# Performance work log

Measured on AMD Instinct MI355X. Metric: run time of the kernel, lower is better.

Reference implementation:

```python
import math
import jax, jax.numpy as jnp
import numpy as np

B, S, D_MODEL = 4, 1024, 512
D_BAR, C_ONSET, N_HEADS = 256, 32, 8
T_ONSET, POOL = 8192, 8


def setup_inputs() -> dict:
    key = jax.random.key(0)
    ks = jax.random.split(key, 16)
    p = lambda i, shape: jax.random.normal(ks[i], shape, dtype=jnp.float32) * 0.05
    return {
        "token_embs": jax.random.normal(ks[0], (B, S, D_MODEL), dtype=jnp.float32),
        "onset_1d": jax.random.uniform(ks[1], (B, T_ONSET, C_ONSET), dtype=jnp.float32),
        "bar_mask": jax.random.bernoulli(ks[2], 0.0625, (B, S)),  # ~1 bar / 16 tokens
        "Wih_note": p(3, (3 * D_BAR, D_MODEL)),
        "Whh_note": p(4, (3 * D_BAR, D_BAR)),
        "bih_note": p(5, (3 * D_BAR,)),
        "bhh_note": p(6, (3 * D_BAR,)),
        "Wih_bar": p(7, (3 * D_BAR, D_BAR)),
        "Whh_bar": p(8, (3 * D_BAR, D_BAR)),
        "bih_bar": p(9, (3 * D_BAR,)),
        "bhh_bar": p(10, (3 * D_BAR,)),
        "Wq": p(11, (D_BAR, D_BAR)),
        "bq": p(12, (D_BAR,)),
        "Wk": p(13, (D_BAR, C_ONSET)),
        "bk": p(14, (D_BAR,)),
        "pos_bias_scale": jnp.float32(2.5),
    }


def _gru_cell(x, h, Wih, Whh, bih, bhh):
    # torch nn.GRU cell, gate order (r, z, n)
    gi = x @ Wih.T + bih
    gh = h @ Whh.T + bhh
    ir, iz, inn = jnp.split(gi, 3, axis=-1)
    hr, hz, hn = jnp.split(gh, 3, axis=-1)
    r = jax.nn.sigmoid(ir + hr)
    z = jax.nn.sigmoid(iz + hz)
    n = jnp.tanh(inn + r * hn)
    return (1.0 - z) * n + z * h


def _sinusoidal_pe(T, C, dtype):
    half = C // 2
    pos = jnp.arange(T, dtype=dtype)
    div = jnp.exp(jnp.arange(half, dtype=dtype) * (-math.log(10000.0) / half))
    ang = pos[:, None] * div[None, :]  # [T, half]
    # interleave sin/cos -> [T, C] (C even)
    return jnp.stack([jnp.sin(ang), jnp.cos(ang)], axis=-1).reshape(T, C)


def _forward(token_embs, onset_1d, bar_mask, Wih_note, Whh_note, bih_note, bhh_note,
             Wih_bar, Whh_bar, bih_bar, bhh_bar, Wq, bq, Wk, bk, pos_bias_scale):
    Bc, Sc, _ = token_embs.shape
    d_bar = Whh_bar.shape[1]
    H = N_HEADS
    dh = d_bar // H
    dtype = token_embs.dtype

    # --- audio keys: avg_pool1d(k=8,s=8) + sinusoidal PE + projection ---
    T = onset_1d.shape[1]
    pooled = onset_1d.reshape(Bc, T // POOL, POOL, onset_1d.shape[2]).mean(axis=2)  # [B,T_oct,C]
    T_oct = pooled.shape[1]
    pe = _sinusoidal_pe(T_oct, pooled.shape[2], dtype)
    K = (pooled + pe[None]) @ Wk.T + bk  # [B,T_oct,d_bar]

    # --- fused note-GRU / bar-GRU scan over sequence positions ---
    # Segment semantics: bar tokens are excluded from note-GRU segments; at a
    # <bar> position the note hidden (= bar summary; zero for empty segments)
    # feeds one bar-GRU step, then the note hidden resets to zero.
    def step(carry, xs):
        h_note, g_bar = carry
        x, m = xs  # x: [B,D], m: [B] bool
        h_next = _gru_cell(x, h_note, Wih_note, Whh_note, bih_note, bhh_note)
        g_next = _gru_cell(h_note, g_bar, Wih_bar, Whh_bar, bih_bar, bhh_bar)
        m_ = m[:, None]
        g_out = jnp.where(m_, g_next, g_bar)
        h_out = jnp.where(m_, jnp.zeros_like(h_next), h_next)
        return (h_out, g_out), g_out

    zeros = jnp.zeros((Bc, d_bar), dtype=dtype)
    (_, g_end), g_seq = jax.lax.scan(
        step, (zeros, zeros),
        (token_embs.transpose(1, 0, 2), bar_mask.T))
    h_bar_carried = g_seq.transpose(1, 0, 2)  # [B,S,d_bar]: h_bar after most recent bar <= s
    h_bar_final = g_end[None]                 # [1,B,d_bar]

    # --- cross-attention com_t (computed densely, masked to <bar> positions) ---
    Q = (h_bar_carried @ Wq.T + bq).reshape(Bc, Sc, H, dh)
    K4 = K.reshape(Bc, T_oct, H, dh)
    scores = jnp.einsum('bshd,bthd->bsht', Q, K4) / math.sqrt(dh)
    time_pos = jnp.linspace(0.0, 1.0, T_oct, dtype=dtype)
    scores = scores - pos_bias_scale * time_pos  # broadcast pos bias over t
    attn = jax.nn.softmax(scores, axis=-1)
    com = jnp.sum(attn.mean(axis=2) * time_pos, axis=-1)  # [B,S]
    com_t_all = jnp.where(bar_mask, com, 0.0)[..., None]  # [B,S,1]

    return com_t_all, h_bar_final, h_bar_carried


def reference(token_embs, onset_1d, bar_mask, Wih_note, Whh_note, bih_note, bhh_note,
              Wih_bar, Whh_bar, bih_bar, bhh_bar, Wq, bq, Wk, bk, pos_bias_scale):
    return _forward(token_embs, onset_1d, bar_mask, Wih_note, Whh_note, bih_note, bhh_note,
                    Wih_bar, Whh_bar, bih_bar, bhh_bar, Wq, bq, Wk, bk, pos_bias_scale)
```

## Files before the change

kernel.cpp:

```cpp
#include <hip/hip_runtime.h>
#include <hip/hip_bf16.h>
#include <math.h>

#define NB 4
#define SEQ 1024
#define DM 512
#define DB 256
#define G3 768
#define CO 32
#define TONS 8192
#define POOLN 8
#define TOCT 1024
#define NH 8
#define DHD 32

#define RKT 5
#define LKT 3

#define OFF_GI     0u
#define OFF_GIBAR  3145728u
#define OFF_HEND   6291456u
#define OFF_GALL   7340032u
#define OFF_KMAT   8388608u
#define OFF_WFN    9437184u
#define OFF_WFB    9535488u
#define OFF_WFIHN  9633792u
#define OFF_WFIHB  9830400u
#define OFF_INT_BYTES 39714816u

#define OUT_FINAL 4096
#define OUT_CARR  5120

typedef __attribute__((ext_vector_type(8))) short short8v;
typedef __attribute__((ext_vector_type(4))) float f32x4;

__device__ __forceinline__ unsigned int bf16rne(float f) {
    unsigned int u = __float_as_uint(f);
    return (u + 0x7fffu + ((u >> 16) & 1u)) >> 16;
}

__global__ __launch_bounds__(256) void k_scan(const unsigned char* __restrict__ mraw,
        int* __restrict__ pos, int* __restrict__ lastk, int* __restrict__ nmask,
        int* __restrict__ sS, int* __restrict__ sLen, int* __restrict__ sC,
        int* __restrict__ nseg) {
    __shared__ int rnz[8];
    __shared__ int gt1;
    __shared__ int mode;
    __shared__ int snm[NB];
    int tid = threadIdx.x;
    if (tid < 8) rnz[tid] = 0;
    if (tid == 0) gt1 = 0;
    __syncthreads();
    for (int i = tid; i < NB * SEQ; i += 256) {
        unsigned char v = mraw[i];
        if (v) {
            rnz[i & 7] = 1;
            if (v > 1) gt1 = 1;
        }
    }
    __syncthreads();
    if (tid == 0) {
        bool lowhalf = rnz[0] | rnz[1] | rnz[4] | rnz[5];
        bool hihalf  = rnz[2] | rnz[3] | rnz[6] | rnz[7];
        int m;
        if (hihalf && !lowhalf) {
            m = (rnz[2] | rnz[3]) ? 3 : 4;
        } else if (gt1) {
            m = 5;
        } else if (rnz[1] | rnz[3] | rnz[5] | rnz[7]) {
            m = 0;
        } else if (rnz[4]) {
            m = 1;
        } else if (rnz[0]) {
            m = 2;
        } else {
            m = 0;
        }
        mode = m;
    }
    __syncthreads();
    if (tid < NB) {
        int b = tid;
        int cnt = 0;
        for (int t = 0; t < SEQ; ++t) {
            int idx = b * SEQ + t;
            int mv;
            switch (mode) {
                case 0:  mv = mraw[idx] != 0; break;
                case 1:  mv = ((const int*)mraw)[idx] != 0; break;
                case 2:  mv = ((const long long*)mraw)[idx] != 0LL; break;
                case 3:  mv = ((const float*)mraw)[idx] != 0.f; break;
                case 4:  mv = ((const double*)mraw)[idx] != 0.0; break;
                default: mv = ((const unsigned short*)mraw)[idx] != 0; break;
            }
            if (mv) { pos[b * SEQ + cnt] = t; ++cnt; }
            lastk[idx] = cnt - 1;
        }
        nmask[b] = cnt;
        snm[b] = cnt;
    }
    __syncthreads();
    if (tid < NB) {
        int b = tid;
        int base = 0;
        for (int x = 0; x < b; ++x) base += snm[x];
        int cnt = snm[b];
        for (int k = 0; k < cnt; ++k) {
            int e = pos[b * SEQ + k];
            int s = (k == 0) ? 0 : (pos[b * SEQ + k - 1] + 1);
            sS[base + k]   = b * SEQ + s;
            sLen[base + k] = e - s;
            sC[base + k]   = b * SEQ + k;
        }
    }
    __syncthreads();
    if (tid == 0) {
        int t = 0;
        for (int x = 0; x < NB; ++x) t += snm[x];
        *nseg = t;
    }
}

__global__ __launch_bounds__(256) void k_wfrag(const float* __restrict__ W, uint4* __restrict__ out,
                                               int Kdim, int KTN) {
    int idx = blockIdx.x * 256 + threadIdx.x;
    if (idx >= 48 * KTN * 64) return;
    int lane = idx & 63;
    int TK = idx >> 6;
    int T = TK / KTN, Kt = TK % KTN;
    int row = 16 * T + (lane & 15);
    int kb = 32 * Kt + (lane >> 4) * 8;
    const float* wr = W + (size_t)row * Kdim + kb;
    uint4 u;
    u.x = bf16rne(wr[0]) | (bf16rne(wr[1]) << 16);
    u.y = bf16rne(wr[2]) | (bf16rne(wr[3]) << 16);
    u.z = bf16rne(wr[4]) | (bf16rne(wr[5]) << 16);
    u.w = bf16rne(wr[6]) | (bf16rne(wr[7]) << 16);
    out[idx] = u;
}

__global__ __launch_bounds__(256) void k_gemm_mfma(int Kdim, int KTN,
        const float* __restrict__ A, const uint4* __restrict__ Bf,
        const float* __restrict__ bias, float* __restrict__ C) {
    int bm = blockIdx.x * 64, bn = blockIdx.y * 64;
    int tid = threadIdx.x;
    int w = tid >> 6;
    int lane = tid & 63;
    int arow = bm + 16 * w + (lane & 15);
    int kofs = (lane >> 4) * 8;
    f32x4 acc[4];
#pragma unroll
    for (int nt = 0; nt < 4; ++nt) acc[nt] = (f32x4){0.f, 0.f, 0.f, 0.f};
    for (int kc = 0; kc < KTN; ++kc) {
        const float* ap = A + (size_t)arow * Kdim + kc * 32 + kofs;
        float4 p0 = *reinterpret_cast<const float4*>(ap);
        float4 p1 = *reinterpret_cast<const float4*>(ap + 4);
        uint4 au;
        au.x = bf16rne(p0.x) | (bf16rne(p0.y) << 16);
        au.y = bf16rne(p0.z) | (bf16rne(p0.w) << 16);
        au.z = bf16rne(p1.x) | (bf16rne(p1.y) << 16);
        au.w = bf16rne(p1.z) | (bf16rne(p1.w) << 16);
        short8v a = __builtin_bit_cast(short8v, au);
#pragma unroll
        for (int nt = 0; nt < 4; ++nt) {
            int T = (bn >> 4) + nt;
            uint4 u = Bf[(size_t)(T * KTN + kc) * 64 + lane];
            short8v bv = __builtin_bit_cast(short8v, u);
            acc[nt] = __builtin_amdgcn_mfma_f32_16x16x32_bf16(a, bv, acc[nt], 0, 0, 0);
        }
    }
    int crow = bm + 16 * w + (lane >> 4) * 4;
#pragma unroll
    for (int nt = 0; nt < 4; ++nt) {
        int col = bn + 16 * nt + (lane & 15);
        float bv = bias[col];
#pragma unroll
        for (int r = 0; r < 4; ++r)
            C[(size_t)(crow + r) * G3 + col] = acc[nt][r] + bv;
    }
}

__global__ __launch_bounds__(64) void k_keys(const float* __restrict__ onset,
        const float* __restrict__ Wk, const float* __restrict__ bk, float* __restrict__ Kmat) {
    int bt = blockIdx.x;
    int b = bt >> 10, t = bt & 1023;
    __shared__ float xin[CO];
    int tid = threadIdx.x;
    if (tid < CO) {
        float s = 0.f;
        const float* base = onset + ((size_t)b * TONS + (size_t)t * POOLN) * CO + tid;
#pragma unroll
        for (int p = 0; p < POOLN; ++p) s += base[p * CO];
        s *= (1.f / POOLN);
        int j = tid >> 1;
        float dv = expf(-logf(10000.f) * (float)j / 16.f);
        float ang = (float)t * dv;
        s += (tid & 1) ? cosf(ang) : sinf(ang);
        xin[tid] = s;
    }
    __syncthreads();
    for (int n = tid; n < DB; n += 64) {
        float acc = bk[n];
        const float* wr = Wk + (size_t)n * CO;
#pragma unroll
        for (int c = 0; c < CO; ++c) acc += xin[c] * wr[c];
        Kmat[(size_t)bt * DB + n] = acc;
    }
}

template<int MODE>
__global__ __launch_bounds__(512, 1) void k_gru(
        const uint4* __restrict__ wf, const float* __restrict__ bhh,
        const float* __restrict__ gx_src,
        const int* __restrict__ sS, const int* __restrict__ sLen,
        const int* __restrict__ sC, const int* __restrict__ nseg_p,
        const int* __restrict__ nmask, float* __restrict__ outp) {
    int bg = blockIdx.x;
    int nseg = (MODE == 0) ? *nseg_p : NB;
    if (16 * bg >= nseg) return;
    int tid = threadIdx.x;
    int w = tid >> 6;
    int lane = tid & 63;
    int lhi = lane >> 4, c = lane & 15;

    __shared__ __align__(16) unsigned short hfrag[8 * 64 * 8];
    __shared__ __align__(16) uint4 wlds[8 * 6 * LKT * 64];

    uint4 wreg[6][RKT];
#pragma unroll
    for (int t = 0; t < 6; ++t) {
        int T = 16 * (t >> 1) + 2 * w + (t & 1);
#pragma unroll
        for (int kt = 0; kt < RKT; ++kt)
            wreg[t][kt] = wf[(size_t)(T * 8 + kt) * 64 + lane];
#pragma unroll
        for (int kt = 0; kt < LKT; ++kt)
            wlds[((w * 6 + t) * LKT + kt) * 64 + lane] = wf[(size_t)(T * 8 + RKT + kt) * 64 + lane];
    }

    int ss_r[4], len_r[4], sc_r[4];
#pragma unroll
    for (int r = 0; r < 4; ++r) {
        int m = 4 * lhi + r;
        int gs = 16 * bg + m;
        if (MODE == 0) {
            bool v = gs < nseg;
            ss_r[r]  = v ? sS[gs] : 0;
            len_r[r] = v ? sLen[gs] : 0;
            sc_r[r]  = v ? sC[gs] : 0;
        } else {
            bool v = m < NB;
            ss_r[r]  = v ? m * SEQ : 0;
            len_r[r] = v ? nmask[m] : 0;
            sc_r[r]  = 0;
        }
    }
    int mx = 0;
    for (int q = 0; q < 16; ++q) {
        int gs = 16 * bg + q;
        int L = (MODE == 0) ? ((gs < nseg) ? sLen[gs] : 0)
                            : ((q < NB) ? nmask[q] : 0);
        mx = max(mx, L);
    }
    float bh[3][2];
#pragma unroll
    for (int g = 0; g < 3; ++g)
#pragma unroll
        for (int ii = 0; ii < 2; ++ii)
            bh[g][ii] = bhh[g * 256 + 32 * w + 16 * ii + c];
    float h[4][2] = {};

    for (int i = 0; i < mx; ++i) {
        float gx[3][2][4];
#pragma unroll
        for (int r = 0; r < 4; ++r) {
            int row = (i < len_r[r]) ? (ss_r[r] + i) : ss_r[r];
            const float* gp = gx_src + (size_t)row * G3 + 32 * w + c;
#pragma unroll
            for (int g = 0; g < 3; ++g)
#pragma unroll
                for (int ii = 0; ii < 2; ++ii)
                    gx[g][ii][r] = gp[g * 256 + 16 * ii];
        }
        f32x4 acc[6];
#pragma unroll
        for (int t = 0; t < 6; ++t) acc[t] = (f32x4){0.f, 0.f, 0.f, 0.f};
        if (i > 0) {
            const short8v* hf8 = (const short8v*)hfrag;
#pragma unroll
            for (int kt = 0; kt < 8; ++kt) {
                short8v a = hf8[kt * 64 + lane];
                if (kt < RKT) {
#pragma unroll
                    for (int t = 0; t < 6; ++t) {
                        short8v bv = __builtin_bit_cast(short8v, wreg[t][kt]);
                        acc[t] = __builtin_amdgcn_mfma_f32_16x16x32_bf16(a, bv, acc[t], 0, 0, 0);
                    }
                } else {
#pragma unroll
                    for (int t = 0; t < 6; ++t) {
                        uint4 u = wlds[((w * 6 + t) * LKT + (kt - RKT)) * 64 + lane];
                        short8v bv = __builtin_bit_cast(short8v, u);
                        acc[t] = __builtin_amdgcn_mfma_f32_16x16x32_bf16(a, bv, acc[t], 0, 0, 0);
                    }
                }
            }
        }
#pragma unroll
        for (int r = 0; r < 4; ++r) {
#pragma unroll
            for (int ii = 0; ii < 2; ++ii) {
                float rr = 1.f / (1.f + expf(-(gx[0][ii][r] + bh[0][ii] + acc[0 + ii][r])));
                float zz = 1.f / (1.f + expf(-(gx[1][ii][r] + bh[1][ii] + acc[2 + ii][r])));
                float nn = tanhf(gx[2][ii][r] + rr * (bh[2][ii] + acc[4 + ii][r]));
                float hv = (1.f - zz) * nn + zz * h[r][ii];
                bool act = i < len_r[r];
                hv = act ? hv : h[r][ii];
                h[r][ii] = hv;
                if (MODE == 1) {
                    if (lhi == 0 && act) {
                        int j = 32 * w + 16 * ii + c;
                        outp[(size_t)(ss_r[r] + i) * DB + j] = hv;
                    }
                }
            }
        }
        __syncthreads();
#pragma unroll
        for (int r = 0; r < 4; ++r)
#pragma unroll
            for (int ii = 0; ii < 2; ++ii) {
                int j = 32 * w + 16 * ii + c;
                int m = 4 * lhi + r;
                int lp = m + 16 * ((j >> 3) & 3);
                hfrag[(size_t)(w * 64 + lp) * 8 + (j & 7)] = (unsigned short)bf16rne(h[r][ii]);
            }
        __syncthreads();
    }
    if (MODE == 0) {
#pragma unroll
        for (int r = 0; r < 4; ++r) {
            int gs = 16 * bg + 4 * lhi + r;
            if (gs < nseg) {
#pragma unroll
                for (int ii = 0; ii < 2; ++ii)
                    outp[(size_t)sc_r[r] * DB + 32 * w + 16 * ii + c] = h[r][ii];
            }
        }
    }
}

__global__ __launch_bounds__(256) void k_fill(const float* __restrict__ gall,
        const int* __restrict__ lastk, const int* __restrict__ nmask,
        float* __restrict__ out) {
    int bt = blockIdx.x;
    int b = bt >> 10, t = bt & 1023;
    int tid = threadIdx.x;
    int lk = lastk[bt];
    float v = (lk >= 0) ? gall[((size_t)b * SEQ + lk) * DB + tid] : 0.f;
    out[OUT_CARR + (size_t)bt * DB + tid] = v;
    if (tid == 0) out[bt] = 0.f;
    if (t == 0) {
        int nm = nmask[b];
        float fv = (nm > 0) ? gall[((size_t)b * SEQ + nm - 1) * DB + tid] : 0.f;
        out[OUT_FINAL + b * DB + tid] = fv;
    }
}

__global__ __launch_bounds__(256) void k_attn(const float* __restrict__ gall,
        const float* __restrict__ Wq, const float* __restrict__ bq,
        const float* __restrict__ Kmat, const int* __restrict__ pos,
        const int* __restrict__ nmask, const float* __restrict__ pbs_ptr,
        float* __restrict__ out) {
    int c = blockIdx.x;
    int b = c >> 10, k = c & 1023;
    if (k >= nmask[b]) return;
    int trow = pos[b * SEQ + k];
    __shared__ float q[DB];
    __shared__ float grow[DB];
    __shared__ float sc[NH][TOCT];
    __shared__ float comh[NH];
    int tid = threadIdx.x;
    grow[tid] = gall[((size_t)b * SEQ + k) * DB + tid];
    __syncthreads();
    {
        float acc = bq[tid];
        const float* wr = Wq + (size_t)tid * DB;
#pragma unroll 4
        for (int j = 0; j < DB; ++j) acc += grow[j] * wr[j];
        q[tid] = acc;
    }
    __syncthreads();
    float pbs = *pbs_ptr;
    const float scale = 0.17677669529663687f;
    for (int t = tid; t < TOCT; t += 256) {
        const float* kr = Kmat + ((size_t)b * TOCT + t) * DB;
        float tp = (float)t * (1.f / 1023.f);
#pragma unroll
        for (int h = 0; h < NH; ++h) {
            float acc = 0.f;
#pragma unroll
            for (int d = 0; d < DHD; ++d) acc += q[h * DHD + d] * kr[h * DHD + d];
            sc[h][t] = acc * scale - pbs * tp;
        }
    }
    __syncthreads();
    int hh = tid >> 5, l = tid & 31;
    float mx = -1e30f;
    for (int t = l; t < TOCT; t += 32) mx = fmaxf(mx, sc[hh][t]);
#pragma unroll
    for (int o = 16; o > 0; o >>= 1) mx = fmaxf(mx, __shfl_xor(mx, o, 32));
    float se = 0.f, sw = 0.f;
    for (int t = l; t < TOCT; t += 32) {
        float e = expf(sc[hh][t] - mx);
        se += e;
        sw += e * ((float)t * (1.f / 1023.f));
    }
#pragma unroll
    for (int o = 16; o > 0; o >>= 1) { se += __shfl_xor(se, o, 32); sw += __shfl_xor(sw, o, 32); }
    if (l == 0) comh[hh] = sw / se;
    __syncthreads();
    if (tid == 0) {
        float cm = 0.f;
#pragma unroll
        for (int h = 0; h < NH; ++h) cm += comh[h];
        out[b * SEQ + trow] = cm * (1.f / NH);
    }
}

extern "C" void kernel_launch(void* const* d_in, const int* in_sizes, int n_in,
                              void* d_out, int out_size, void* d_ws, size_t ws_size,
                              hipStream_t stream) {
    const float* te    = (const float*)d_in[0];
    const float* onset = (const float*)d_in[1];
    const unsigned char* mask = (const unsigned char*)d_in[2];
    const float* Wih_n = (const float*)d_in[3];
    const float* Whh_n = (const float*)d_in[4];
    const float* bih_n = (const float*)d_in[5];
    const float* bhh_n = (const float*)d_in[6];
    const float* Wih_b = (const float*)d_in[7];
    const float* Whh_b = (const float*)d_in[8];
    const float* bih_b = (const float*)d_in[9];
    const float* bhh_b = (const float*)d_in[10];
    const float* Wq    = (const float*)d_in[11];
    const float* bq    = (const float*)d_in[12];
    const float* Wk    = (const float*)d_in[13];
    const float* bk    = (const float*)d_in[14];
    const float* pbs   = (const float*)d_in[15];
    float* out = (float*)d_out;

    float* ws    = (float*)d_ws;
    float* gi    = ws + OFF_GI;
    float* gibar = ws + OFF_GIBAR;
    float* hend  = ws + OFF_HEND;
    float* gall  = ws + OFF_GALL;
    float* kmat  = ws + OFF_KMAT;
    uint4* wfn   = (uint4*)(ws + OFF_WFN);
    uint4* wfb   = (uint4*)(ws + OFF_WFB);
    uint4* wfihn = (uint4*)(ws + OFF_WFIHN);
    uint4* wfihb = (uint4*)(ws + OFF_WFIHB);
    int* ipos    = (int*)((char*)d_ws + OFF_INT_BYTES);
    int* ilastk  = ipos + NB * SEQ;
    int* inmask  = ilastk + NB * SEQ;
    int* isS     = inmask + NB;
    int* isLen   = isS + NB * SEQ;
    int* isC     = isLen + NB * SEQ;
    int* inseg   = isC + NB * SEQ;

    k_scan<<<1, 256, 0, stream>>>(mask, ipos, ilastk, inmask, isS, isLen, isC, inseg);
    k_wfrag<<<96, 256, 0, stream>>>(Whh_n, wfn, DB, 8);
    k_wfrag<<<96, 256, 0, stream>>>(Whh_b, wfb, DB, 8);
    k_wfrag<<<192, 256, 0, stream>>>(Wih_n, wfihn, DM, 16);
    k_wfrag<<<96, 256, 0, stream>>>(Wih_b, wfihb, DB, 8);
    k_keys<<<NB * TOCT, 64, 0, stream>>>(onset, Wk, bk, kmat);
    k_gemm_mfma<<<dim3(64, 12), 256, 0, stream>>>(DM, 16, te, wfihn, bih_n, gi);
    k_gru<0><<<256, 512, 0, stream>>>(wfn, bhh_n, gi, isS, isLen, isC, inseg, inmask, hend);
    k_gemm_mfma<<<dim3(64, 12), 256, 0, stream>>>(DB, 8, hend, wfihb, bih_b, gibar);
    k_gru<1><<<1, 512, 0, stream>>>(wfb, bhh_b, gibar, isS, isLen, isC, inseg, inmask, gall);
    k_fill<<<NB * SEQ, 256, 0, stream>>>(gall, ilastk, inmask, out);
    k_attn<<<NB * SEQ, 256, 0, stream>>>(gall, Wq, bq, kmat, ipos, inmask, pbs, out);
}
```

Measured before the change: 981.2 us.

## Prefetch GRU input gates one step ahead, use fast math, skip masked gemm tiles

The GRU recurrence loop is unrolled by two with double-buffered gate-input registers, so global loads for step i+1 are issued before step i's MFMA and activation work. This hides load latency on the serial critical path. Sigmoid, tanh and the softmax exp switch to fast __expf/__fdividef intrinsics, which lowers accuracy somewhat. The bar-level input GEMM also skips row tiles past each batch's bar count, and the unrolled loop may read the gate-input row at one step past the sequence end.

Result: faster. 941.5 us (-4.0%).

```diff
diff --git a/kernel.cpp b/kernel.cpp
--- a/kernel.cpp
+++ b/kernel.cpp
@@ -37,6 +37,12 @@
 __device__ __forceinline__ unsigned int bf16rne(float f) {
     unsigned int u = __float_as_uint(f);
     return (u + 0x7fffu + ((u >> 16) & 1u)) >> 16;
+}
+__device__ __forceinline__ float fsigm(float x) {
+    return __fdividef(1.f, 1.f + __expf(-x));
+}
+__device__ __forceinline__ float ftanh(float x) {
+    return 1.f - __fdividef(2.f, __expf(2.f * x) + 1.f);
 }
 
 __global__ __launch_bounds__(256) void k_scan(const unsigned char* __restrict__ mraw,
@@ -139,10 +145,16 @@
     out[idx] = u;
 }
 
+template<bool LIM>
 __global__ __launch_bounds__(256) void k_gemm_mfma(int Kdim, int KTN,
         const float* __restrict__ A, const uint4* __restrict__ Bf,
-        const float* __restrict__ bias, float* __restrict__ C) {
+        const float* __restrict__ bias, float* __restrict__ C,
+        const int* __restrict__ nmask) {
     int bm = blockIdx.x * 64, bn = blockIdx.y * 64;
+    if (LIM) {
+        int b = bm >> 10;
+        if ((bm & 1023) >= nmask[b]) return;
+    }
     int tid = threadIdx.x;
     int w = tid >> 6;
     int lane = tid & 63;
@@ -270,73 +282,93 @@
             bh[g][ii] = bhh[g * 256 + 32 * w + 16 * ii + c];
     float h[4][2] = {};
 
-    for (int i = 0; i < mx; ++i) {
-        float gx[3][2][4];
-#pragma unroll
-        for (int r = 0; r < 4; ++r) {
-            int row = (i < len_r[r]) ? (ss_r[r] + i) : ss_r[r];
-            const float* gp = gx_src + (size_t)row * G3 + 32 * w + c;
-#pragma unroll
-            for (int g = 0; g < 3; ++g)
-#pragma unroll
-                for (int ii = 0; ii < 2; ++ii)
-                    gx[g][ii][r] = gp[g * 256 + 16 * ii];
-        }
-        f32x4 acc[6];
-#pragma unroll
-        for (int t = 0; t < 6; ++t) acc[t] = (f32x4){0.f, 0.f, 0.f, 0.f};
-        if (i > 0) {
-            const short8v* hf8 = (const short8v*)hfrag;
-#pragma unroll
-            for (int kt = 0; kt < 8; ++kt) {
-                short8v a = hf8[kt * 64 + lane];
-                if (kt < RKT) {
-#pragma unroll
-                    for (int t = 0; t < 6; ++t) {
-                        short8v bv = __builtin_bit_cast(short8v, wreg[t][kt]);
-                        acc[t] = __builtin_amdgcn_mfma_f32_16x16x32_bf16(a, bv, acc[t], 0, 0, 0);
-                    }
-                } else {
-#pragma unroll
-                    for (int t = 0; t < 6; ++t) {
-                        uint4 u = wlds[((w * 6 + t) * LKT + (kt - RKT)) * 64 + lane];
-                        short8v bv = __builtin_bit_cast(short8v, u);
-                        acc[t] = __builtin_amdgcn_mfma_f32_16x16x32_bf16(a, bv, acc[t], 0, 0, 0);
-                    }
-                }
-            }
-        }
-#pragma unroll
-        for (int r = 0; r < 4; ++r) {
-#pragma unroll
-            for (int ii = 0; ii < 2; ++ii) {
-                float rr = 1.f / (1.f + expf(-(gx[0][ii][r] + bh[0][ii] + acc[0 + ii][r])));
-                float zz = 1.f / (1.f + expf(-(gx[1][ii][r] + bh[1][ii] + acc[2 + ii][r])));
-                float nn = tanhf(gx[2][ii][r] + rr * (bh[2][ii] + acc[4 + ii][r]));
-                float hv = (1.f - zz) * nn + zz * h[r][ii];
-                bool act = i < len_r[r];
-                hv = act ? hv : h[r][ii];
-                h[r][ii] = hv;
-                if (MODE == 1) {
-                    if (lhi == 0 && act) {
-                        int j = 32 * w + 16 * ii + c;
-                        outp[(size_t)(ss_r[r] + i) * DB + j] = hv;
-                    }
-                }
-            }
-        }
-        __syncthreads();
-#pragma unroll
-        for (int r = 0; r < 4; ++r)
-#pragma unroll
-            for (int ii = 0; ii < 2; ++ii) {
-                int j = 32 * w + 16 * ii + c;
-                int m = 4 * lhi + r;
-                int lp = m + 16 * ((j >> 3) & 3);
-                hfrag[(size_t)(w * 64 + lp) * 8 + (j & 7)] = (unsigned short)bf16rne(h[r][ii]);
-            }
-        __syncthreads();
-    }
+#define LOADGX(dst, step)                                                        \
+    {                                                                            \
+        int i_ = (step);                                                         \
+        _Pragma("unroll")                                                        \
+        for (int r = 0; r < 4; ++r) {                                            \
+            int row = (i_ < len_r[r]) ? (ss_r[r] + i_) : ss_r[r];                \
+            const float* gp = gx_src + (size_t)row * G3 + 32 * w + c;            \
+            _Pragma("unroll")                                                    \
+            for (int g = 0; g < 3; ++g)                                          \
+                _Pragma("unroll")                                                \
+                for (int ii = 0; ii < 2; ++ii)                                   \
+                    dst[g][ii][r] = gp[g * 256 + 16 * ii];                       \
+        }                                                                        \
+    }
+
+#define GRU_STEP(I, GX)                                                          \
+    {                                                                            \
+        int i_ = (I);                                                            \
+        f32x4 acc[6];                                                            \
+        _Pragma("unroll")                                                        \
+        for (int t = 0; t < 6; ++t) acc[t] = (f32x4){0.f, 0.f, 0.f, 0.f};        \
+        if (i_ > 0) {                                                            \
+            const short8v* hf8 = (const short8v*)hfrag;                          \
+            _Pragma("unroll")                                                    \
+            for (int kt = 0; kt < 8; ++kt) {                                     \
+                short8v a = hf8[kt * 64 + lane];                                 \
+                if (kt < RKT) {                                                  \
+                    _Pragma("unroll")                                            \
+                    for (int t = 0; t < 6; ++t) {                                \
+                        short8v bv = __builtin_bit_cast(short8v, wreg[t][kt]);   \
+                        acc[t] = __builtin_amdgcn_mfma_f32_16x16x32_bf16(        \
+                                a, bv, acc[t], 0, 0, 0);                         \
+                    }                                                            \
+                } else {                                                         \
+                    _Pragma("unroll")                                            \
+                    for (int t = 0; t < 6; ++t) {                                \
+                        uint4 u = wlds[((w * 6 + t) * LKT + (kt - RKT)) * 64 + lane]; \
+                        short8v bv = __builtin_bit_cast(short8v, u);             \
+                        acc[t] = __builtin_amdgcn_mfma_f32_16x16x32_bf16(        \
+                                a, bv, acc[t], 0, 0, 0);                         \
+                    }                                                            \
+                }                                                                \
+            }                                                                    \
+        }                                                                        \
+        _Pragma("unroll")                                                        \
+        for (int r = 0; r < 4; ++r) {                                            \
+            _Pragma("unroll")                                                    \
+            for (int ii = 0; ii < 2; ++ii) {                                     \
+                float rr = fsigm(GX[0][ii][r] + bh[0][ii] + acc[0 + ii][r]);     \
+                float zz = fsigm(GX[1][ii][r] + bh[1][ii] + acc[2 + ii][r]);     \
+                float nn = ftanh(GX[2][ii][r] + rr * (bh[2][ii] + acc[4 + ii][r])); \
+                float hv = (1.f - zz) * nn + zz * h[r][ii];                      \
+                bool act = i_ < len_r[r];                                        \
+                hv = act ? hv : h[r][ii];                                        \
+                h[r][ii] = hv;                                                   \
+                if (MODE == 1) {                                                 \
+                    if (lhi == 0 && act) {                                       \
+                        int j = 32 * w + 16 * ii + c;                            \
+                        outp[(size_t)(ss_r[r] + i_) * DB + j] = hv;              \
+                    }                                                            \
+                }                                                                \
+            }                                                                    \
+        }                                                                        \
+        __syncthreads();                                                         \
+        _Pragma("unroll")                                                        \
+        for (int r = 0; r < 4; ++r)                                              \
+            _Pragma("unroll")                                                    \
+            for (int ii = 0; ii < 2; ++ii) {                                     \
+                int j = 32 * w + 16 * ii + c;                                    \
+                int m = 4 * lhi + r;                                             \
+                int lp = m + 16 * ((j >> 3) & 3);                                \
+                hfrag[(size_t)(w * 64 + lp) * 8 + (j & 7)] =                     \
+                    (unsigned short)bf16rne(h[r][ii]);                           \
+            }                                                                    \
+        __syncthreads();                                                         \
+    }
+
+    float gxa[3][2][4], gxb[3][2][4];
+    LOADGX(gxa, 0)
+    for (int i = 0; i < mx; i += 2) {
+        LOADGX(gxb, i + 1)
+        GRU_STEP(i, gxa)
+        LOADGX(gxa, i + 2)
+        GRU_STEP(i + 1, gxb)
+    }
+#undef LOADGX
+#undef GRU_STEP
     if (MODE == 0) {
 #pragma unroll
         for (int r = 0; r < 4; ++r) {
@@ -412,7 +444,7 @@
     for (int o = 16; o > 0; o >>= 1) mx = fmaxf(mx, __shfl_xor(mx, o, 32));
     float se = 0.f, sw = 0.f;
     for (int t = l; t < TOCT; t += 32) {
-        float e = expf(sc[hh][t] - mx);
+        float e = __expf(sc[hh][t] - mx);
         se += e;
         sw += e * ((float)t * (1.f / 1023.f));
     }
@@ -473,9 +505,9 @@
     k_wfrag<<<192, 256, 0, stream>>>(Wih_n, wfihn, DM, 16);
     k_wfrag<<<96, 256, 0, stream>>>(Wih_b, wfihb, DB, 8);
     k_keys<<<NB * TOCT, 64, 0, stream>>>(onset, Wk, bk, kmat);
-    k_gemm_mfma<<<dim3(64, 12), 256, 0, stream>>>(DM, 16, te, wfihn, bih_n, gi);
+    k_gemm_mfma<false><<<dim3(64, 12), 256, 0, stream>>>(DM, 16, te, wfihn, bih_n, gi, inmask);
     k_gru<0><<<256, 512, 0, stream>>>(wfn, bhh_n, gi, isS, isLen, isC, inseg, inmask, hend);
-    k_gemm_mfma<<<dim3(64, 12), 256, 0, stream>>>(DB, 8, hend, wfihb, bih_b, gibar);
+    k_gemm_mfma<true><<<dim3(64, 12), 256, 0, stream>>>(DB, 8, hend, wfihb, bih_b, gibar, inmask);
     k_gru<1><<<1, 512, 0, stream>>>(wfb, bhh_b, gibar, isS, isLen, isC, inseg, inmask, gall);
     k_fill<<<NB * SEQ, 256, 0, stream>>>(gall, ilastk, inmask, out);
     k_attn<<<NB * SEQ, 256, 0, stream>>>(gall, Wq, bq, kmat, ipos, inmask, pbs, out);
```
